# Performance work log

Measured on AMD Instinct MI355X. Metric: run time of the kernel, lower is better.

Reference implementation:

```python
import jax, jax.numpy as jnp
import numpy as np

N, E, H, L = 20000, 640000, 128, 3
IN_NODE, IN_EDGE = 128, 128


def _ln(x):
    m = jnp.mean(x, -1, keepdims=True)
    v = jnp.mean((x - m) ** 2, -1, keepdims=True)
    return (x - m) / jnp.sqrt(v + 1e-5)


def _multi_aggr(msg, dst, n):
    # PyG MultiAggregation(['mean','std','max','min']) -> concat on feature dim
    cnt = jax.ops.segment_sum(jnp.ones((msg.shape[0],), msg.dtype), dst, n)
    denom = jnp.maximum(cnt, 1.0)[:, None]
    mean = jax.ops.segment_sum(msg, dst, n) / denom
    mean2 = jax.ops.segment_sum(msg * msg, dst, n) / denom
    std = jnp.sqrt(jax.nn.relu(mean2 - mean * mean) + 1e-5)  # PyG StdAggregation
    has = (cnt > 0)[:, None]
    mx = jnp.where(has, jax.ops.segment_max(msg, dst, n), 0.0)
    mn = jnp.where(has, jax.ops.segment_min(msg, dst, n), 0.0)
    return jnp.concatenate([mean, std, mx, mn], axis=-1)  # [n, 4H]


def _pna(h, src, dst, ea, W1, b1, W2, b2, W3, b3, W4, b4, Wd, bd, n):
    # flow='source_to_target': j = src = edge_index[0], i = dst = edge_index[1]
    x1 = jax.nn.silu(h @ W1 + b1)  # lin1 -> x_j
    z = jax.nn.silu(h @ W2 + b2)   # lin2 -> z_i
    msg = z[dst] * x1[src] * ea    # message = z_i * x_j * edge_attr
    ret_node = _multi_aggr(msg, dst, n) @ Wd + bd
    ret_edge = jax.nn.silu(h @ W3 + b3)[src] * jax.nn.silu(h @ W4 + b4)[dst] * ea
    return ret_node, ret_edge


def _gnn(x, edge_index, edge_attr, Wn, bn, We, be, W1, b1, W2, b2, W3, b3, W4, b4,
         Wd, bd, Wnd1, bnd1, Wnd2, bnd2, Wed1, bed1, Wed2, bed2):
    n = x.shape[0]
    h = Wn.shape[1]
    src, dst = edge_index[0], edge_index[1]
    inv = jnp.concatenate([jnp.ones((h // 2,), x.dtype), -jnp.ones(((h + 1) // 2,), x.dtype)])
    hidden = x @ Wn + bn
    in_ea = edge_attr
    ea = edge_attr @ We + be
    for i in range(W1.shape[0]):
        hn = _ln(hidden)
        rn1, re1 = _pna(hn, src, dst, ea, W1[i], b1[i], W2[i], b2[i], W3[i], b3[i], W4[i], b4[i], Wd[i], bd[i], n)
        rn2, re2 = _pna(hn, dst, src, inv * ea, W1[i], b1[i], W2[i], b2[i], W3[i], b3[i], W4[i], b4[i], Wd[i], bd[i], n)
        hidden = hidden + rn1 + rn2
        ea = ea + re1 + inv * re2
    node_pred = x + 0.01 * (jax.nn.silu(_ln(hidden) @ Wnd1 + bnd1) @ Wnd2 + bnd2)
    edge_pred = in_ea + 0.01 * (jax.nn.silu(_ln(ea) @ Wed1 + bed1) @ Wed2 + bed2)
    return node_pred, edge_pred


def setup_inputs() -> dict:
    key = jax.random.key(0)
    ks = jax.random.split(key, 20)
    g = lambda k, s, sc=0.05: jax.random.normal(k, s, jnp.float32) * sc
    return {
        "x": g(ks[0], (N, IN_NODE), 1.0),
        "edge_attr": g(ks[1], (E, IN_EDGE), 1.0),
        "Wn": g(ks[2], (IN_NODE, H)), "bn": jnp.zeros((H,), jnp.float32),
        "We": g(ks[3], (IN_EDGE, H)), "be": jnp.zeros((H,), jnp.float32),
        "W1": g(ks[4], (L, H, H)), "b1": jnp.zeros((L, H), jnp.float32),
        "W2": g(ks[5], (L, H, H)), "b2": jnp.zeros((L, H), jnp.float32),
        "W3": g(ks[6], (L, H, H)), "b3": jnp.zeros((L, H), jnp.float32),
        "W4": g(ks[7], (L, H, H)), "b4": jnp.zeros((L, H), jnp.float32),
        "Wd": g(ks[8], (L, 4 * H, H)), "bd": jnp.zeros((L, H), jnp.float32),
        "Wnd1": g(ks[9], (H, H)), "bnd1": jnp.zeros((H,), jnp.float32),
        "Wnd2": g(ks[10], (H, IN_NODE)), "bnd2": jnp.zeros((IN_NODE,), jnp.float32),
        "Wed1": g(ks[11], (H, H)), "bed1": jnp.zeros((H,), jnp.float32),
        "Wed2": g(ks[12], (H, IN_EDGE)), "bed2": jnp.zeros((IN_EDGE,), jnp.float32),
        "edge_index": jax.random.randint(ks[13], (2, E), 0, N),
    }


def reference(x, edge_attr, Wn, bn, We, be, W1, b1, W2, b2, W3, b3, W4, b4, Wd, bd,
              Wnd1, bnd1, Wnd2, bnd2, Wed1, bed1, Wed2, bed2, edge_index):
    return _gnn(x, edge_index, edge_attr, Wn, bn, We, be, W1, b1, W2, b2, W3, b3,
                W4, b4, Wd, bd, Wnd1, bnd1, Wnd2, bnd2, Wed1, bed1, Wed2, bed2)
```

## Files before the change

kernel.cpp:

```cpp
#include <hip/hip_runtime.h>
#include <cstdint>
#include <cstddef>

typedef __attribute__((ext_vector_type(8))) short short8x;
typedef __attribute__((ext_vector_type(4))) float f32x4;
typedef __attribute__((ext_vector_type(4))) unsigned int u32x4;

static constexpr int NN = 20000;
static constexpr int EE = 640000;
static constexpr int NT_E = EE / 128;

#define DEVI __device__ __forceinline__

DEVI float b2f(uint16_t u){ union{uint32_t i; float f;} x; x.i = (uint32_t)u<<16; return x.f; }
DEVI uint16_t f2b(float f){ union{float f; uint32_t i;} x; x.f=f; uint32_t i=x.i;
  return (uint16_t)((i + 0x7FFFu + ((i>>16)&1u))>>16); }
DEVI float silu_f(float v){ return v / (1.f + __expf(-v)); }

DEVI uint4 pack8(float4 a, float4 b){
  union{uint16_t u[8]; uint4 q;} pk;
  pk.u[0]=f2b(a.x); pk.u[1]=f2b(a.y); pk.u[2]=f2b(a.z); pk.u[3]=f2b(a.w);
  pk.u[4]=f2b(b.x); pk.u[5]=f2b(b.y); pk.u[6]=f2b(b.z); pk.u[7]=f2b(b.w);
  return pk.q;
}
DEVI uint2 pack4(float4 a){
  union{uint16_t u[4]; uint2 q;} pk;
  pk.u[0]=f2b(a.x); pk.u[1]=f2b(a.y); pk.u[2]=f2b(a.z); pk.u[3]=f2b(a.w);
  return pk.q;
}
DEVI float4 unpk4(uint2 v){
  return (float4){ b2f((uint16_t)(v.x & 0xFFFFu)), b2f((uint16_t)(v.x >> 16)),
                   b2f((uint16_t)(v.y & 0xFFFFu)), b2f((uint16_t)(v.y >> 16)) };
}
DEVI short8x pk_frag(float4 a, float4 b){
  union{uint16_t u[8]; short8x s;} pk;
  pk.u[0]=f2b(a.x); pk.u[1]=f2b(a.y); pk.u[2]=f2b(a.z); pk.u[3]=f2b(a.w);
  pk.u[4]=f2b(b.x); pk.u[5]=f2b(b.y); pk.u[6]=f2b(b.z); pk.u[7]=f2b(b.w);
  return pk.s;
}

DEVI float4 ntld4f(const float* p){
  f32x4 v = __builtin_nontemporal_load((const f32x4*)p);
  return (float4){v.x, v.y, v.z, v.w};
}

template<typename EAT>
DEVI void load8e(const EAT* base, size_t row, int col8, float4& a, float4& b){
  if constexpr (sizeof(EAT)==2){
    uint4 v = *(const uint4*)((const uint16_t*)base + row*128 + col8);
    a = (float4){b2f((uint16_t)(v.x&0xFFFFu)), b2f((uint16_t)(v.x>>16)),
                 b2f((uint16_t)(v.y&0xFFFFu)), b2f((uint16_t)(v.y>>16))};
    b = (float4){b2f((uint16_t)(v.z&0xFFFFu)), b2f((uint16_t)(v.z>>16)),
                 b2f((uint16_t)(v.w&0xFFFFu)), b2f((uint16_t)(v.w>>16))};
  } else {
    const float* f = (const float*)base + row*128 + col8;
    a = *(const float4*)f; b = *(const float4*)(f+4);
  }
}
template<typename EAT>
DEVI void store4e(EAT* base, size_t idx, float4 v){
  if constexpr (sizeof(EAT)==2) *(uint2*)((uint16_t*)base + idx) = pack4(v);
  else *(float4*)((float*)base + idx) = v;
}
template<typename EAT>
DEVI float4 ld4e(const EAT* base, size_t idx){
  if constexpr (sizeof(EAT)==2) return unpk4(*(const uint2*)((const uint16_t*)base + idx));
  else return *(const float4*)((const float*)base + idx);
}

DEVI void ln8(float4& a, float4& b){
  float s = a.x+a.y+a.z+a.w + b.x+b.y+b.z+b.w;
  float q = a.x*a.x+a.y*a.y+a.z*a.z+a.w*a.w + b.x*b.x+b.y*b.y+b.z*b.z+b.w*b.w;
#pragma unroll
  for (int d=1; d<16; d<<=1){ s += __shfl_xor(s,d); q += __shfl_xor(q,d); }
  float m = s * 0.0078125f;
  float rstd = rsqrtf(fmaxf(q*0.0078125f - m*m, 0.f) + 1e-5f);
  a.x=(a.x-m)*rstd; a.y=(a.y-m)*rstd; a.z=(a.z-m)*rstd; a.w=(a.w-m)*rstd;
  b.x=(b.x-m)*rstd; b.y=(b.y-m)*rstd; b.z=(b.z-m)*rstd; b.w=(b.w-m)*rstd;
}

template<int AF32, int LNA, int EPI, int SILU>
__global__ __launch_bounds__(256) void gemm_node(
    const void* Ap, const uint16_t* __restrict__ Wt,
    const float* __restrict__ bias, float bias_scale,
    int M, int K,
    uint16_t* outb, float* outf,
    const float* __restrict__ resid, float resid_scale)
{
  __shared__ uint16_t Als[128*136];
  __shared__ uint16_t Wls[128*136];
  const int t = threadIdx.x;
  const int row0 = blockIdx.x * 128;
  const int w = t >> 6, l = t & 63;
  const int lr = l & 15, lk = (l>>4)*8;

  f32x4 acc[2][8];
#pragma unroll
  for (int a=0;a<2;a++)
#pragma unroll
    for(int b=0;b<8;b++) acc[a][b] = (f32x4){0.f,0.f,0.f,0.f};

  for (int kc = 0; kc < K; kc += 128){
#pragma unroll
    for (int i=0;i<8;i++){
      int c = t + i*256;
      int r = c >> 4, k8 = (c & 15)*8;
      int gr = row0 + r;
      if (AF32){
        float4 a = {0.f,0.f,0.f,0.f}, b = {0.f,0.f,0.f,0.f};
        if (gr < M){
          const float* Af = (const float*)Ap + (size_t)gr*K + kc + k8;
          a = *(const float4*)Af; b = *(const float4*)(Af + 4);
        }
        if (LNA) ln8(a, b);
        *(uint4*)(&Als[r*136 + k8]) = pack8(a, b);
      } else {
        uint4 v = {0u,0u,0u,0u};
        if (gr < M) v = *(const uint4*)((const uint16_t*)Ap + (size_t)gr*K + kc + k8);
        *(uint4*)(&Als[r*136 + k8]) = v;
      }
    }
#pragma unroll
    for (int i=0;i<8;i++){
      int c = t + i*256;
      int r = c >> 4, k8 = (c & 15)*8;
      *(uint4*)(&Wls[r*136 + k8]) = *(const uint4*)(Wt + (size_t)r*K + kc + k8);
    }
    __syncthreads();
#pragma unroll
    for (int kt=0; kt<4; ++kt){
      int kb = kt*32 + lk;
      short8x bfr[8];
#pragma unroll
      for (int c16=0;c16<8;c16++) bfr[c16] = *(const short8x*)(&Wls[(c16*16+lr)*136 + kb]);
#pragma unroll
      for (int r16=0;r16<2;r16++){
        short8x afr = *(const short8x*)(&Als[(w*32 + r16*16 + lr)*136 + kb]);
#pragma unroll
        for (int c16=0;c16<8;c16++)
          acc[r16][c16] = __builtin_amdgcn_mfma_f32_16x16x32_bf16(bfr[c16], afr, acc[r16][c16], 0,0,0);
      }
    }
    __syncthreads();
  }

  float4 bbv[8];
#pragma unroll
  for (int c16=0;c16<8;c16++){
    float4 b4 = *(const float4*)(bias + c16*16 + (l>>4)*4);
    bbv[c16] = (float4){b4.x*bias_scale, b4.y*bias_scale, b4.z*bias_scale, b4.w*bias_scale};
  }
#pragma unroll
  for (int r16=0;r16<2;r16++){
    int row = row0 + w*32 + r16*16 + lr;
    if (row >= M) continue;
#pragma unroll
    for (int c16=0;c16<8;c16++){
      int colb = c16*16 + (l>>4)*4;
      float4 v = (float4){acc[r16][c16][0]+bbv[c16].x, acc[r16][c16][1]+bbv[c16].y,
                          acc[r16][c16][2]+bbv[c16].z, acc[r16][c16][3]+bbv[c16].w};
      if (SILU){ v.x=silu_f(v.x); v.y=silu_f(v.y); v.z=silu_f(v.z); v.w=silu_f(v.w); }
      size_t o = (size_t)row*128 + colb;
      if (EPI==0)      *(uint2*)(outb + o) = pack4(v);
      else if (EPI==1) *(float4*)(outf + o) = v;
      else if (EPI==2){ float4 old = *(const float4*)(outf + o);
        *(float4*)(outf + o) = (float4){old.x+v.x, old.y+v.y, old.z+v.z, old.w+v.w}; }
      else { float4 r = *(const float4*)(resid + o);
        *(float4*)(outf + o) = (float4){r.x+resid_scale*v.x, r.y+resid_scale*v.y,
                                        r.z+resid_scale*v.z, r.w+resid_scale*v.w}; }
    }
  }
}

__global__ __launch_bounds__(256) void proj4(
    const float* __restrict__ hidden, const uint16_t* __restrict__ Wt4,
    const float* __restrict__ b0p, const float* __restrict__ b1p,
    const float* __restrict__ b2p, const float* __restrict__ b3p,
    uint16_t* o0, uint16_t* o1, uint16_t* o2, uint16_t* o3, int M)
{
  __shared__ uint16_t Als[128*136];
  __shared__ uint16_t Wls[2][128*136];
  const int t = threadIdx.x;
  const int row0 = blockIdx.x * 128;
  const int w = t >> 6, l = t & 63;
  const int lr = l & 15, lk = (l>>4)*8;

#pragma unroll
  for (int i=0;i<8;i++){
    int c = t + i*256;
    int r = c >> 4, k8 = (c & 15)*8;
    int gr = row0 + r;
    float4 a = {0.f,0.f,0.f,0.f}, b = {0.f,0.f,0.f,0.f};
    if (gr < M){
      const float* Af = hidden + (size_t)gr*128 + k8;
      a = *(const float4*)Af; b = *(const float4*)(Af + 4);
    }
    ln8(a, b);
    *(uint4*)(&Als[r*136 + k8]) = pack8(a, b);
  }
#pragma unroll
  for (int i=0;i<8;i++){
    int c = t + i*256;
    int r = c >> 4, k8 = (c & 15)*8;
    *(uint4*)(&Wls[0][r*136 + k8]) = *(const uint4*)(Wt4 + (size_t)r*128 + k8);
  }
  __syncthreads();

#pragma unroll
  for (int p=0; p<4; ++p){
    if (p < 3){
#pragma unroll
      for (int i=0;i<8;i++){
        int c = t + i*256;
        int r = c >> 4, k8 = (c & 15)*8;
        *(uint4*)(&Wls[(p+1)&1][r*136 + k8]) =
          *(const uint4*)(Wt4 + (size_t)(p+1)*16384 + (size_t)r*128 + k8);
      }
    }
    f32x4 acc[2][8];
#pragma unroll
    for (int a=0;a<2;a++)
#pragma unroll
      for(int b=0;b<8;b++) acc[a][b] = (f32x4){0.f,0.f,0.f,0.f};
#pragma unroll
    for (int kt=0; kt<4; ++kt){
      int kb = kt*32 + lk;
      short8x bfr[8];
#pragma unroll
      for (int c16=0;c16<8;c16++) bfr[c16] = *(const short8x*)(&Wls[p&1][(c16*16+lr)*136 + kb]);
#pragma unroll
      for (int r16=0;r16<2;r16++){
        short8x afr = *(const short8x*)(&Als[(w*32 + r16*16 + lr)*136 + kb]);
#pragma unroll
        for (int c16=0;c16<8;c16++)
          acc[r16][c16] = __builtin_amdgcn_mfma_f32_16x16x32_bf16(bfr[c16], afr, acc[r16][c16], 0,0,0);
      }
    }
    const float* bp = (p==0)?b0p:(p==1)?b1p:(p==2)?b2p:b3p;
    uint16_t* op = (p==0)?o0:(p==1)?o1:(p==2)?o2:o3;
#pragma unroll
    for (int r16=0;r16<2;r16++){
      int row = row0 + w*32 + r16*16 + lr;
      if (row >= M) continue;
#pragma unroll
      for (int c16=0;c16<8;c16++){
        int colb = c16*16 + (l>>4)*4;
        float4 b4 = *(const float4*)(bp + colb);
        float4 v = (float4){silu_f(acc[r16][c16][0]+b4.x), silu_f(acc[r16][c16][1]+b4.y),
                            silu_f(acc[r16][c16][2]+b4.z), silu_f(acc[r16][c16][3]+b4.w)};
        *(uint2*)(op + (size_t)row*128 + colb) = pack4(v);
      }
    }
    __syncthreads();
  }
}

template<typename EAT>
__global__ __launch_bounds__(256, 2) void enc_edge(
    const float* __restrict__ A, const uint16_t* __restrict__ Wt,
    const float* __restrict__ bias, EAT* __restrict__ out)
{
  const int t = threadIdx.x, w = t >> 6, l = t & 63;
  const int lr = l & 15, g = l >> 4;

  float4 bbv[8];
#pragma unroll
  for (int c16=0;c16<8;c16++) bbv[c16] = *(const float4*)(bias + c16*16 + g*4);

  int tile = blockIdx.x;
  float4 va[16];
#pragma unroll
  for (int r16=0;r16<2;r16++)
#pragma unroll
    for (int kt=0;kt<4;kt++){
      const float* Af = A + ((size_t)tile*128 + w*32 + r16*16 + lr)*128 + kt*32 + g*8;
      va[r16*8+kt*2]   = ntld4f(Af);
      va[r16*8+kt*2+1] = ntld4f(Af + 4);
    }
  while (tile < NT_E){
    short8x fr[2][4];
#pragma unroll
    for (int r16=0;r16<2;r16++)
#pragma unroll
      for (int kt=0;kt<4;kt++)
        fr[r16][kt] = pk_frag(va[r16*8+kt*2], va[r16*8+kt*2+1]);
    int next = tile + (int)gridDim.x;
    if (next < NT_E){
#pragma unroll
      for (int r16=0;r16<2;r16++)
#pragma unroll
        for (int kt=0;kt<4;kt++){
          const float* Af = A + ((size_t)next*128 + w*32 + r16*16 + lr)*128 + kt*32 + g*8;
          va[r16*8+kt*2]   = ntld4f(Af);
          va[r16*8+kt*2+1] = ntld4f(Af + 4);
        }
    }
    f32x4 acc[2][8];
#pragma unroll
    for (int a=0;a<2;a++)
#pragma unroll
      for (int b=0;b<8;b++) acc[a][b] = (f32x4){0.f,0.f,0.f,0.f};
#pragma unroll
    for (int kt=0;kt<4;kt++){
#pragma unroll
      for (int c16=0;c16<8;c16++){
        short8x bfr = *(const short8x*)(Wt + (size_t)(c16*16+lr)*128 + kt*32 + g*8);
        acc[0][c16] = __builtin_amdgcn_mfma_f32_16x16x32_bf16(bfr, fr[0][kt], acc[0][c16], 0,0,0);
        acc[1][c16] = __builtin_amdgcn_mfma_f32_16x16x32_bf16(bfr, fr[1][kt], acc[1][c16], 0,0,0);
      }
    }
#pragma unroll
    for (int r16=0;r16<2;r16++){
      size_t row = (size_t)tile*128 + w*32 + r16*16 + lr;
#pragma unroll
      for (int c16=0;c16<8;c16++){
        int colb = c16*16 + g*4;
        store4e(out, row*128 + colb,
          (float4){acc[r16][c16][0]+bbv[c16].x, acc[r16][c16][1]+bbv[c16].y,
                   acc[r16][c16][2]+bbv[c16].z, acc[r16][c16][3]+bbv[c16].w});
      }
    }
    tile = next;
  }
}

template<typename EAT>
__global__ __launch_bounds__(256, 2) void dec_edge(
    const EAT* ea, const float* __restrict__ eatt,
    const uint16_t* __restrict__ W1t, const uint16_t* __restrict__ W2t,
    const float* __restrict__ b1, const float* __restrict__ b2,
    float* outf)
{
  __shared__ uint16_t Pls[4][32*136];
  const int t = threadIdx.x, w = t >> 6, l = t & 63;
  const int lr = l & 15, g = l >> 4;
  uint16_t* Ps = &Pls[w][0];
  const size_t base = (size_t)blockIdx.x*128 + w*32;

  float4 et[16];
#pragma unroll
  for (int r16=0;r16<2;r16++){
    size_t row = base + r16*16 + lr;
#pragma unroll
    for (int c16=0;c16<8;c16++)
      et[r16*8+c16] = *(const float4*)(eatt + row*128 + c16*16 + g*4);
  }

  short8x fr[2][4];
#pragma unroll
  for (int r16=0;r16<2;r16++){
    float4 va[4][2];
    float s=0.f, q=0.f;
#pragma unroll
    for (int kt=0;kt<4;kt++){
      load8e(ea, base + r16*16 + lr, kt*32 + g*8, va[kt][0], va[kt][1]);
      float4 a = va[kt][0], b = va[kt][1];
      s += a.x+a.y+a.z+a.w + b.x+b.y+b.z+b.w;
      q += a.x*a.x+a.y*a.y+a.z*a.z+a.w*a.w + b.x*b.x+b.y*b.y+b.z*b.z+b.w*b.w;
    }
    s += __shfl_xor(s,16); q += __shfl_xor(q,16);
    s += __shfl_xor(s,32); q += __shfl_xor(q,32);
    float m = s*0.0078125f;
    float rstd = rsqrtf(fmaxf(q*0.0078125f - m*m, 0.f) + 1e-5f);
#pragma unroll
    for (int kt=0;kt<4;kt++){
      float4 a = va[kt][0], b = va[kt][1];
      a.x=(a.x-m)*rstd; a.y=(a.y-m)*rstd; a.z=(a.z-m)*rstd; a.w=(a.w-m)*rstd;
      b.x=(b.x-m)*rstd; b.y=(b.y-m)*rstd; b.z=(b.z-m)*rstd; b.w=(b.w-m)*rstd;
      fr[r16][kt] = pk_frag(a, b);
    }
  }
  f32x4 acc[2][8];
#pragma unroll
  for (int a=0;a<2;a++)
#pragma unroll
    for (int b=0;b<8;b++) acc[a][b] = (f32x4){0.f,0.f,0.f,0.f};
#pragma unroll
  for (int kt=0;kt<4;kt++){
#pragma unroll
    for (int c16=0;c16<8;c16++){
      short8x bfr = *(const short8x*)(W1t + (size_t)(c16*16+lr)*128 + kt*32 + g*8);
      acc[0][c16] = __builtin_amdgcn_mfma_f32_16x16x32_bf16(fr[0][kt], bfr, acc[0][c16], 0,0,0);
      acc[1][c16] = __builtin_amdgcn_mfma_f32_16x16x32_bf16(fr[1][kt], bfr, acc[1][c16], 0,0,0);
    }
  }
#pragma unroll
  for (int c16=0;c16<8;c16++){
    float bb = b1[c16*16+lr];
#pragma unroll
    for (int r16=0;r16<2;r16++)
#pragma unroll
      for (int j=0;j<4;j++)
        Ps[(r16*16 + g*4 + j)*136 + c16*16 + lr] = f2b(silu_f(acc[r16][c16][j] + bb));
  }
  f32x4 acc2[2][8];
#pragma unroll
  for (int a=0;a<2;a++)
#pragma unroll
    for (int b=0;b<8;b++) acc2[a][b] = (f32x4){0.f,0.f,0.f,0.f};
#pragma unroll
  for (int kt=0;kt<4;kt++){
    short8x a0 = *(const short8x*)(Ps + (0*16 + lr)*136 + kt*32 + g*8);
    short8x a1 = *(const short8x*)(Ps + (1*16 + lr)*136 + kt*32 + g*8);
#pragma unroll
    for (int c16=0;c16<8;c16++){
      short8x bfr = *(const short8x*)(W2t + (size_t)(c16*16+lr)*128 + kt*32 + g*8);
      acc2[0][c16] = __builtin_amdgcn_mfma_f32_16x16x32_bf16(bfr, a0, acc2[0][c16], 0,0,0);
      acc2[1][c16] = __builtin_amdgcn_mfma_f32_16x16x32_bf16(bfr, a1, acc2[1][c16], 0,0,0);
    }
  }
#pragma unroll
  for (int r16=0;r16<2;r16++){
    size_t row = base + r16*16 + lr;
#pragma unroll
    for (int c16=0;c16<8;c16++){
      int colb = c16*16 + g*4;
      float4 bb = *(const float4*)(b2 + colb);
      float4 e = et[r16*8+c16];
      *(float4*)(outf + row*128 + colb) =
        (float4){e.x + 0.01f*(acc2[r16][c16][0]+bb.x),
                 e.y + 0.01f*(acc2[r16][c16][1]+bb.y),
                 e.z + 0.01f*(acc2[r16][c16][2]+bb.z),
                 e.w + 0.01f*(acc2[r16][c16][3]+bb.w)};
    }
  }
}

template<typename EAT, int INV, int EUPD, int ACCUM>
__global__ __launch_bounds__(128) void agg_kernel(
    const EAT* ea, EAT* ea_out,
    const uint16_t* __restrict__ x1, const uint16_t* __restrict__ z,
    const uint16_t* __restrict__ h3, const uint16_t* __restrict__ h4,
    const int* __restrict__ eids, const int* __restrict__ ptr,
    const int* __restrict__ other, uint16_t* stats)
{
  __shared__ int se[128];
  __shared__ int so[128];
  __shared__ float red[4][4][128];
  const int i = blockIdx.x, t = threadIdx.x;
  const int g = t >> 5, q = t & 31;
  const int f0 = q*4;
  float4 zi = unpk4(*(const uint2*)(z + (size_t)i*128 + f0));
  float4 h3i = {0,0,0,0}, h4i = {0,0,0,0};
  if (EUPD){
    h3i = unpk4(*(const uint2*)(h3 + (size_t)i*128 + f0));
    h4i = unpk4(*(const uint2*)(h4 + (size_t)i*128 + f0));
  }
  const int beg = ptr[i], end = ptr[i+1];
  float4 s={0,0,0,0}, s2={0,0,0,0};
  float4 mx={-3.4e38f,-3.4e38f,-3.4e38f,-3.4e38f}, mn={3.4e38f,3.4e38f,3.4e38f,3.4e38f};
  for (int jb = beg; jb < end; jb += 128){
    int cn = min(128, end - jb);
    if (t < cn){ int e = eids[jb+t]; se[t] = e; so[t] = other[e]; }
    __syncthreads();
#pragma unroll 4
    for (int jj = g; jj < cn; jj += 4){
      int e = se[jj], o = so[jj];
      float4 xo = unpk4(*(const uint2*)(x1 + (size_t)o*128 + f0));
      float4 ev = ld4e(ea, (size_t)e*128 + f0);
      float4 m = (float4){zi.x*xo.x*ev.x, zi.y*xo.y*ev.y, zi.z*xo.z*ev.z, zi.w*xo.w*ev.w};
      if (INV){ if (q >= 16){ m.x=-m.x; m.y=-m.y; m.z=-m.z; m.w=-m.w; } }
      s.x+=m.x; s.y+=m.y; s.z+=m.z; s.w+=m.w;
      s2.x+=m.x*m.x; s2.y+=m.y*m.y; s2.z+=m.z*m.z; s2.w+=m.w*m.w;
      mx.x=fmaxf(mx.x,m.x); mx.y=fmaxf(mx.y,m.y); mx.z=fmaxf(mx.z,m.z); mx.w=fmaxf(mx.w,m.w);
      mn.x=fminf(mn.x,m.x); mn.y=fminf(mn.y,m.y); mn.z=fminf(mn.z,m.z); mn.w=fminf(mn.w,m.w);
      if (EUPD){
        float4 h3o = unpk4(*(const uint2*)(h3 + (size_t)o*128 + f0));
        float4 h4o = unpk4(*(const uint2*)(h4 + (size_t)o*128 + f0));
        store4e(ea_out, (size_t)e*128 + f0,
          (float4){ev.x*(1.f + h3o.x*h4i.x + h3i.x*h4o.x),
                   ev.y*(1.f + h3o.y*h4i.y + h3i.y*h4o.y),
                   ev.z*(1.f + h3o.z*h4i.z + h3i.z*h4o.z),
                   ev.w*(1.f + h3o.w*h4i.w + h3i.w*h4o.w)});
      }
    }
    __syncthreads();
  }
  *(float4*)(&red[g][0][f0]) = s;
  *(float4*)(&red[g][1][f0]) = s2;
  *(float4*)(&red[g][2][f0]) = mx;
  *(float4*)(&red[g][3][f0]) = mn;
  __syncthreads();
  float fs = red[0][0][t]+red[1][0][t]+red[2][0][t]+red[3][0][t];
  float fq = red[0][1][t]+red[1][1][t]+red[2][1][t]+red[3][1][t];
  float fmx = fmaxf(fmaxf(red[0][2][t],red[1][2][t]), fmaxf(red[2][2][t],red[3][2][t]));
  float fmn = fminf(fminf(red[0][3][t],red[1][3][t]), fminf(red[2][3][t],red[3][3][t]));
  int cnt = end - beg;
  float dn = cnt > 0 ? 1.f/(float)cnt : 1.f;
  float mean = fs*dn, m2 = fq*dn;
  float sd = sqrtf(fmaxf(m2 - mean*mean, 0.f) + 1e-5f);
  if (cnt == 0){ fmx = 0.f; fmn = 0.f; }
  size_t o0 = (size_t)i*512 + t;
  if (ACCUM){
    stats[o0    ] = f2b(b2f(stats[o0    ]) + mean);
    stats[o0+128] = f2b(b2f(stats[o0+128]) + sd);
    stats[o0+256] = f2b(b2f(stats[o0+256]) + fmx);
    stats[o0+384] = f2b(b2f(stats[o0+384]) + fmn);
  } else {
    stats[o0]=f2b(mean); stats[o0+128]=f2b(sd); stats[o0+256]=f2b(fmx); stats[o0+384]=f2b(fmn);
  }
}

__global__ void count_deg(const int* __restrict__ ei, int* cnt_src, int* cnt_dst){
  int e = blockIdx.x*256 + threadIdx.x;
  if (e < EE){
    atomicAdd(&cnt_src[ei[e]], 1);
    atomicAdd(&cnt_dst[ei[EE+e]], 1);
  }
}

__global__ __launch_bounds__(1024) void scan20k(const int* __restrict__ cnt, int* ptr, int* cur){
  __shared__ int buf[1024];
  constexpr int C = 20;
  int t = threadIdx.x;
  int base = t*C;
  int loc[C];
  int sum = 0;
#pragma unroll
  for (int j=0;j<C;j++){
    int idx = base+j;
    int v = (idx < NN) ? cnt[idx] : 0;
    loc[j] = sum; sum += v;
  }
  buf[t] = sum;
  __syncthreads();
  for (int sft=1; sft<1024; sft<<=1){
    int add = (t>=sft) ? buf[t-sft] : 0;
    __syncthreads();
    buf[t] += add;
    __syncthreads();
  }
  int excl = buf[t] - sum;
#pragma unroll
  for (int j=0;j<C;j++){
    int idx = base+j;
    if (idx < NN){ int v = excl + loc[j]; ptr[idx] = v; cur[idx] = v; }
  }
  if (t == 1023) ptr[NN] = buf[1023];
}

__global__ void scatter_edges(const int* __restrict__ ei, int* cur_src, int* cur_dst,
                              int* eid_src, int* eid_dst){
  int e = blockIdx.x*256 + threadIdx.x;
  if (e < EE){
    int s = ei[e], d = ei[EE+e];
    eid_src[atomicAdd(&cur_src[s],1)] = e;
    eid_dst[atomicAdd(&cur_dst[d],1)] = e;
  }
}

struct TD { const float* s; uint16_t* d; int K; int ostride; int ooff; int cum; };
struct TPack { TD td[11]; };
__global__ __launch_bounds__(256) void transpose_all(TPack P, int total){
  int idx = blockIdx.x*256 + threadIdx.x;
  if (idx >= total) return;
  int s = 0;
#pragma unroll
  for (int k=0;k<11;k++) s += (idx >= P.td[k].cum) ? 1 : 0;
  int start = (s==0) ? 0 : P.td[s-1].cum;
  int local = idx - start;
  const TD& D = P.td[s];
  int per = D.K*128;
  int m = local / per, r = local - m*per;
  int k = r >> 7, c = r & 127;
  D.d[(size_t)m*D.ostride + D.ooff + (size_t)c*D.K + k] = f2b(D.s[local]);
}

extern "C" void kernel_launch(void* const* d_in, const int* in_sizes, int n_in,
                              void* d_out, int out_size, void* d_ws, size_t ws_size,
                              hipStream_t stream)
{
  const float* x    = (const float*)d_in[0];
  const float* eatt = (const float*)d_in[1];
  const float* Wn   = (const float*)d_in[2];
  const float* bn   = (const float*)d_in[3];
  const float* We   = (const float*)d_in[4];
  const float* be   = (const float*)d_in[5];
  const float* W1   = (const float*)d_in[6];
  const float* b1   = (const float*)d_in[7];
  const float* W2   = (const float*)d_in[8];
  const float* b2   = (const float*)d_in[9];
  const float* W3   = (const float*)d_in[10];
  const float* b3   = (const float*)d_in[11];
  const float* W4   = (const float*)d_in[12];
  const float* b4   = (const float*)d_in[13];
  const float* Wd   = (const float*)d_in[14];
  const float* bd   = (const float*)d_in[15];
  const float* Wnd1 = (const float*)d_in[16];
  const float* bnd1 = (const float*)d_in[17];
  const float* Wnd2 = (const float*)d_in[18];
  const float* bnd2 = (const float*)d_in[19];
  const float* Wed1 = (const float*)d_in[20];
  const float* bed1 = (const float*)d_in[21];
  const float* Wed2 = (const float*)d_in[22];
  const float* bed2 = (const float*)d_in[23];
  const int* ei     = (const int*)d_in[24];

  float* out_node = (float*)d_out;
  float* out_edge = out_node + (size_t)NN*128;

  char* p = (char*)d_ws;
  auto alloc = [&](size_t bytes)->char*{
    char* r = p; p += (bytes + 255) & ~(size_t)255; return r; };

  float*    hidden = (float*)   alloc((size_t)NN*128*4);
  uint16_t* x1b    = (uint16_t*)alloc((size_t)NN*128*2);
  uint16_t* zb     = (uint16_t*)alloc((size_t)NN*128*2);
  uint16_t* h3b    = (uint16_t*)alloc((size_t)NN*128*2);
  uint16_t* h4b    = (uint16_t*)alloc((size_t)NN*128*2);
  uint16_t* stats  = (uint16_t*)alloc((size_t)NN*512*2);
  int* cnt_src = (int*)alloc((size_t)NN*4);
  int* cnt_dst = (int*)alloc((size_t)NN*4);
  int* ptr_src = (int*)alloc((size_t)(NN+1)*4);
  int* ptr_dst = (int*)alloc((size_t)(NN+1)*4);
  int* cur_src = (int*)alloc((size_t)NN*4);
  int* cur_dst = (int*)alloc((size_t)NN*4);
  int* eid_src = (int*)alloc((size_t)EE*4);
  int* eid_dst = (int*)alloc((size_t)EE*4);
  uint16_t* WT  = (uint16_t*)alloc((size_t)294912*2);
  uint16_t* wp4 = (uint16_t*)alloc((size_t)3*65536*2);

  uint16_t* wnT   = WT;
  uint16_t* weT   = WT + 16384;
  uint16_t* wdT   = WT + 32768;
  uint16_t* wnd1T = WT + 229376;
  uint16_t* wnd2T = WT + 245760;
  uint16_t* wed1T = WT + 262144;
  uint16_t* wed2T = WT + 278528;

  size_t used = (size_t)(p - (char*)d_ws);
  bool ea16ok = (ws_size >= used + (size_t)EE*128*2 + 512);
  uint16_t* ea16 = nullptr;
  if (ea16ok) ea16 = (uint16_t*)alloc((size_t)EE*128*2);
  float* eaf = out_edge;

  hipMemsetAsync(cnt_src, 0, (size_t)NN*4, stream);
  hipMemsetAsync(cnt_dst, 0, (size_t)NN*4, stream);
  count_deg<<<(EE+255)/256, 256, 0, stream>>>(ei, cnt_src, cnt_dst);
  scan20k<<<1, 1024, 0, stream>>>(cnt_src, ptr_src, cur_src);
  scan20k<<<1, 1024, 0, stream>>>(cnt_dst, ptr_dst, cur_dst);
  scatter_edges<<<(EE+255)/256, 256, 0, stream>>>(ei, cur_src, cur_dst, eid_src, eid_dst);

  {
    TPack P;
    int cum = 0;
    auto seg = [&](int idx, const float* s, uint16_t* d, int K, int total, int ostride, int ooff){
      cum += total;
      P.td[idx] = TD{s, d, K, ostride, ooff, cum};
    };
    seg(0,  Wn,   wnT,   128, 16384,  16384, 0);
    seg(1,  We,   weT,   128, 16384,  16384, 0);
    seg(2,  W1,   wp4,   128, 49152,  65536, 0);
    seg(3,  W2,   wp4,   128, 49152,  65536, 16384);
    seg(4,  W3,   wp4,   128, 49152,  65536, 32768);
    seg(5,  W4,   wp4,   128, 49152,  65536, 49152);
    seg(6,  Wd,   wdT,   512, 196608, 65536, 0);
    seg(7,  Wnd1, wnd1T, 128, 16384,  16384, 0);
    seg(8,  Wnd2, wnd2T, 128, 16384,  16384, 0);
    seg(9,  Wed1, wed1T, 128, 16384,  16384, 0);
    seg(10, Wed2, wed2T, 128, 16384,  16384, 0);
    transpose_all<<<(cum+255)/256, 256, 0, stream>>>(P, cum);
  }

  const int gN = (NN+127)/128;

  gemm_node<1,0,1,0><<<gN, 256, 0, stream>>>(x, wnT, bn, 1.f, NN, 128, nullptr, hidden, nullptr, 0.f);

  if (ea16ok){
    enc_edge<uint16_t><<<1000, 256, 0, stream>>>(eatt, weT, be, ea16);
    for (int lyr = 0; lyr < 3; ++lyr){
      proj4<<<gN, 256, 0, stream>>>(hidden, wp4 + (size_t)lyr*65536,
                                    b1 + lyr*128, b2 + lyr*128, b3 + lyr*128, b4 + lyr*128,
                                    x1b, zb, h3b, h4b, NN);
      agg_kernel<uint16_t,1,0,0><<<NN, 128, 0, stream>>>(ea16, nullptr, x1b, zb, nullptr, nullptr,
                                                         eid_src, ptr_src, ei + EE, stats);
      agg_kernel<uint16_t,0,1,1><<<NN, 128, 0, stream>>>(ea16, ea16, x1b, zb, h3b, h4b,
                                                         eid_dst, ptr_dst, ei, stats);
      gemm_node<0,0,2,0><<<gN, 256, 0, stream>>>(stats, wdT + lyr*65536, bd + lyr*128, 2.f,
                                                 NN, 512, nullptr, hidden, nullptr, 0.f);
    }
  } else {
    enc_edge<float><<<1000, 256, 0, stream>>>(eatt, weT, be, eaf);
    for (int lyr = 0; lyr < 3; ++lyr){
      proj4<<<gN, 256, 0, stream>>>(hidden, wp4 + (size_t)lyr*65536,
                                    b1 + lyr*128, b2 + lyr*128, b3 + lyr*128, b4 + lyr*128,
                                    x1b, zb, h3b, h4b, NN);
      agg_kernel<float,1,0,0><<<NN, 128, 0, stream>>>(eaf, nullptr, x1b, zb, nullptr, nullptr,
                                                      eid_src, ptr_src, ei + EE, stats);
      agg_kernel<float,0,1,1><<<NN, 128, 0, stream>>>(eaf, eaf, x1b, zb, h3b, h4b,
                                                      eid_dst, ptr_dst, ei, stats);
      gemm_node<0,0,2,0><<<gN, 256, 0, stream>>>(stats, wdT + lyr*65536, bd + lyr*128, 2.f,
                                                 NN, 512, nullptr, hidden, nullptr, 0.f);
    }
  }

  gemm_node<1,1,0,1><<<gN, 256, 0, stream>>>(hidden, wnd1T, bnd1, 1.f, NN, 128, x1b, nullptr, nullptr, 0.f);
  gemm_node<0,0,3,0><<<gN, 256, 0, stream>>>(x1b, wnd2T, bnd2, 1.f, NN, 128, nullptr, out_node, x, 0.01f);

  if (ea16ok)
    dec_edge<uint16_t><<<NT_E, 256, 0, stream>>>(ea16, eatt, wed1T, wed2T, bed1, bed2, out_edge);
  else
    dec_edge<float><<<NT_E, 256, 0, stream>>>(eaf, eatt, wed1T, wed2T, bed1, bed2, out_edge);
}
```

Baseline: 1.425 ms.

## Make dec_edge persistent with register prefetch of next tile inputs

The edge decoder becomes a grid-stride persistent kernel launched with 1024 blocks instead of one block per 128-edge tile. Each iteration loads the next tile's edge features and edge attributes into registers while the current tile's MFMA GEMMs run, and the biases are hoisted out of the loop. The aim is to hide global load latency and cut block launch overhead. In exchange, register pressure rises from holding prefetched data, which could lower occupancy or cause spills under the 256x2 launch bounds.

```diff
diff --git a/kernel.cpp b/kernel.cpp
--- a/kernel.cpp
+++ b/kernel.cpp
@@ -4,7 +4,6 @@
 
 typedef __attribute__((ext_vector_type(8))) short short8x;
 typedef __attribute__((ext_vector_type(4))) float f32x4;
-typedef __attribute__((ext_vector_type(4))) unsigned int u32x4;
 
 static constexpr int NN = 20000;
 static constexpr int EE = 640000;
@@ -32,6 +31,12 @@
   return (float4){ b2f((uint16_t)(v.x & 0xFFFFu)), b2f((uint16_t)(v.x >> 16)),
                    b2f((uint16_t)(v.y & 0xFFFFu)), b2f((uint16_t)(v.y >> 16)) };
 }
+DEVI void unpk8(uint4 v, float4& a, float4& b){
+  a = (float4){b2f((uint16_t)(v.x&0xFFFFu)), b2f((uint16_t)(v.x>>16)),
+               b2f((uint16_t)(v.y&0xFFFFu)), b2f((uint16_t)(v.y>>16))};
+  b = (float4){b2f((uint16_t)(v.z&0xFFFFu)), b2f((uint16_t)(v.z>>16)),
+               b2f((uint16_t)(v.w&0xFFFFu)), b2f((uint16_t)(v.w>>16))};
+}
 DEVI short8x pk_frag(float4 a, float4 b){
   union{uint16_t u[8]; short8x s;} pk;
   pk.u[0]=f2b(a.x); pk.u[1]=f2b(a.y); pk.u[2]=f2b(a.z); pk.u[3]=f2b(a.w);
@@ -44,19 +49,6 @@
   return (float4){v.x, v.y, v.z, v.w};
 }
 
-template<typename EAT>
-DEVI void load8e(const EAT* base, size_t row, int col8, float4& a, float4& b){
-  if constexpr (sizeof(EAT)==2){
-    uint4 v = *(const uint4*)((const uint16_t*)base + row*128 + col8);
-    a = (float4){b2f((uint16_t)(v.x&0xFFFFu)), b2f((uint16_t)(v.x>>16)),
-                 b2f((uint16_t)(v.y&0xFFFFu)), b2f((uint16_t)(v.y>>16))};
-    b = (float4){b2f((uint16_t)(v.z&0xFFFFu)), b2f((uint16_t)(v.z>>16)),
-                 b2f((uint16_t)(v.w&0xFFFFu)), b2f((uint16_t)(v.w>>16))};
-  } else {
-    const float* f = (const float*)base + row*128 + col8;
-    a = *(const float4*)f; b = *(const float4*)(f+4);
-  }
-}
 template<typename EAT>
 DEVI void store4e(EAT* base, size_t idx, float4 v){
   if constexpr (sizeof(EAT)==2) *(uint2*)((uint16_t*)base + idx) = pack4(v);
@@ -335,94 +327,153 @@
   const int t = threadIdx.x, w = t >> 6, l = t & 63;
   const int lr = l & 15, g = l >> 4;
   uint16_t* Ps = &Pls[w][0];
-  const size_t base = (size_t)blockIdx.x*128 + w*32;
-
+
+  float bb1[8];
+  float4 bb2v[8];
+#pragma unroll
+  for (int c16=0;c16<8;c16++){
+    bb1[c16] = b1[c16*16+lr];
+    bb2v[c16] = *(const float4*)(b2 + c16*16 + g*4);
+  }
+
+  int tile = blockIdx.x;
+  size_t base = (size_t)tile*128 + w*32;
+
+  uint4 eaR[8];
+  float4 eaF[16];
   float4 et[16];
-#pragma unroll
-  for (int r16=0;r16<2;r16++){
-    size_t row = base + r16*16 + lr;
-#pragma unroll
-    for (int c16=0;c16<8;c16++)
-      et[r16*8+c16] = *(const float4*)(eatt + row*128 + c16*16 + g*4);
-  }
-
-  short8x fr[2][4];
-#pragma unroll
-  for (int r16=0;r16<2;r16++){
-    float4 va[4][2];
-    float s=0.f, q=0.f;
+
+  if (tile < NT_E){
+    if constexpr (sizeof(EAT)==2){
+#pragma unroll
+      for (int r16=0;r16<2;r16++)
+#pragma unroll
+        for (int kt=0;kt<4;kt++)
+          eaR[r16*4+kt] = *(const uint4*)((const uint16_t*)ea + (base + r16*16+lr)*128 + kt*32 + g*8);
+    } else {
+#pragma unroll
+      for (int r16=0;r16<2;r16++)
+#pragma unroll
+        for (int kt=0;kt<4;kt++){
+          const float* f = (const float*)ea + (base + r16*16+lr)*128 + kt*32 + g*8;
+          eaF[(r16*4+kt)*2]   = *(const float4*)f;
+          eaF[(r16*4+kt)*2+1] = *(const float4*)(f+4);
+        }
+    }
+#pragma unroll
+    for (int r16=0;r16<2;r16++)
+#pragma unroll
+      for (int c16=0;c16<8;c16++)
+        et[r16*8+c16] = *(const float4*)(eatt + (base + r16*16+lr)*128 + c16*16 + g*4);
+  }
+
+  while (tile < NT_E){
+    short8x fr[2][4];
+#pragma unroll
+    for (int r16=0;r16<2;r16++){
+      float4 va[4][2];
+      float s=0.f, q=0.f;
+#pragma unroll
+      for (int kt=0;kt<4;kt++){
+        if constexpr (sizeof(EAT)==2) unpk8(eaR[r16*4+kt], va[kt][0], va[kt][1]);
+        else { va[kt][0]=eaF[(r16*4+kt)*2]; va[kt][1]=eaF[(r16*4+kt)*2+1]; }
+        float4 a = va[kt][0], b = va[kt][1];
+        s += a.x+a.y+a.z+a.w + b.x+b.y+b.z+b.w;
+        q += a.x*a.x+a.y*a.y+a.z*a.z+a.w*a.w + b.x*b.x+b.y*b.y+b.z*b.z+b.w*b.w;
+      }
+      s += __shfl_xor(s,16); q += __shfl_xor(q,16);
+      s += __shfl_xor(s,32); q += __shfl_xor(q,32);
+      float m = s*0.0078125f;
+      float rstd = rsqrtf(fmaxf(q*0.0078125f - m*m, 0.f) + 1e-5f);
+#pragma unroll
+      for (int kt=0;kt<4;kt++){
+        float4 a = va[kt][0], b = va[kt][1];
+        a.x=(a.x-m)*rstd; a.y=(a.y-m)*rstd; a.z=(a.z-m)*rstd; a.w=(a.w-m)*rstd;
+        b.x=(b.x-m)*rstd; b.y=(b.y-m)*rstd; b.z=(b.z-m)*rstd; b.w=(b.w-m)*rstd;
+        fr[r16][kt] = pk_frag(a, b);
+      }
+    }
+    int next = tile + (int)gridDim.x;
+    size_t nbase = (size_t)next*128 + w*32;
+    if (next < NT_E){
+      if constexpr (sizeof(EAT)==2){
+#pragma unroll
+        for (int r16=0;r16<2;r16++)
+#pragma unroll
+          for (int kt=0;kt<4;kt++)
+            eaR[r16*4+kt] = *(const uint4*)((const uint16_t*)ea + (nbase + r16*16+lr)*128 + kt*32 + g*8);
+      } else {
+#pragma unroll
+        for (int r16=0;r16<2;r16++)
+#pragma unroll
+          for (int kt=0;kt<4;kt++){
+            const float* f = (const float*)ea + (nbase + r16*16+lr)*128 + kt*32 + g*8;
+            eaF[(r16*4+kt)*2]   = *(const float4*)f;
+            eaF[(r16*4+kt)*2+1] = *(const float4*)(f+4);
+          }
+      }
+    }
+    f32x4 acc[2][8];
+#pragma unroll
+    for (int a=0;a<2;a++)
+#pragma unroll
+      for (int b=0;b<8;b++) acc[a][b] = (f32x4){0.f,0.f,0.f,0.f};
 #pragma unroll
     for (int kt=0;kt<4;kt++){
-      load8e(ea, base + r16*16 + lr, kt*32 + g*8, va[kt][0], va[kt][1]);
-      float4 a = va[kt][0], b = va[kt][1];
-      s += a.x+a.y+a.z+a.w + b.x+b.y+b.z+b.w;
-      q += a.x*a.x+a.y*a.y+a.z*a.z+a.w*a.w + b.x*b.x+b.y*b.y+b.z*b.z+b.w*b.w;
-    }
-    s += __shfl_xor(s,16); q += __shfl_xor(q,16);
-    s += __shfl_xor(s,32); q += __shfl_xor(q,32);
-    float m = s*0.0078125f;
-    float rstd = rsqrtf(fmaxf(q*0.0078125f - m*m, 0.f) + 1e-5f);
+#pragma unroll
+      for (int c16=0;c16<8;c16++){
+        short8x bfr = *(const short8x*)(W1t + (size_t)(c16*16+lr)*128 + kt*32 + g*8);
+        acc[0][c16] = __builtin_amdgcn_mfma_f32_16x16x32_bf16(fr[0][kt], bfr, acc[0][c16], 0,0,0);
+        acc[1][c16] = __builtin_amdgcn_mfma_f32_16x16x32_bf16(fr[1][kt], bfr, acc[1][c16], 0,0,0);
+      }
+    }
+#pragma unroll
+    for (int c16=0;c16<8;c16++){
+#pragma unroll
+      for (int r16=0;r16<2;r16++)
+#pragma unroll
+        for (int j=0;j<4;j++)
+          Ps[(r16*16 + g*4 + j)*136 + c16*16 + lr] = f2b(silu_f(acc[r16][c16][j] + bb1[c16]));
+    }
+    f32x4 acc2[2][8];
+#pragma unroll
+    for (int a=0;a<2;a++)
+#pragma unroll
+      for (int b=0;b<8;b++) acc2[a][b] = (f32x4){0.f,0.f,0.f,0.f};
 #pragma unroll
     for (int kt=0;kt<4;kt++){
-      float4 a = va[kt][0], b = va[kt][1];
-      a.x=(a.x-m)*rstd; a.y=(a.y-m)*rstd; a.z=(a.z-m)*rstd; a.w=(a.w-m)*rstd;
-      b.x=(b.x-m)*rstd; b.y=(b.y-m)*rstd; b.z=(b.z-m)*rstd; b.w=(b.w-m)*rstd;
-      fr[r16][kt] = pk_frag(a, b);
-    }
-  }
-  f32x4 acc[2][8];
-#pragma unroll
-  for (int a=0;a<2;a++)
-#pragma unroll
-    for (int b=0;b<8;b++) acc[a][b] = (f32x4){0.f,0.f,0.f,0.f};
-#pragma unroll
-  for (int kt=0;kt<4;kt++){
-#pragma unroll
-    for (int c16=0;c16<8;c16++){
-      short8x bfr = *(const short8x*)(W1t + (size_t)(c16*16+lr)*128 + kt*32 + g*8);
-      acc[0][c16] = __builtin_amdgcn_mfma_f32_16x16x32_bf16(fr[0][kt], bfr, acc[0][c16], 0,0,0);
-      acc[1][c16] = __builtin_amdgcn_mfma_f32_16x16x32_bf16(fr[1][kt], bfr, acc[1][c16], 0,0,0);
-    }
-  }
-#pragma unroll
-  for (int c16=0;c16<8;c16++){
-    float bb = b1[c16*16+lr];
-#pragma unroll
-    for (int r16=0;r16<2;r16++)
-#pragma unroll
-      for (int j=0;j<4;j++)
-        Ps[(r16*16 + g*4 + j)*136 + c16*16 + lr] = f2b(silu_f(acc[r16][c16][j] + bb));
-  }
-  f32x4 acc2[2][8];
-#pragma unroll
-  for (int a=0;a<2;a++)
-#pragma unroll
-    for (int b=0;b<8;b++) acc2[a][b] = (f32x4){0.f,0.f,0.f,0.f};
-#pragma unroll
-  for (int kt=0;kt<4;kt++){
-    short8x a0 = *(const short8x*)(Ps + (0*16 + lr)*136 + kt*32 + g*8);
-    short8x a1 = *(const short8x*)(Ps + (1*16 + lr)*136 + kt*32 + g*8);
-#pragma unroll
-    for (int c16=0;c16<8;c16++){
-      short8x bfr = *(const short8x*)(W2t + (size_t)(c16*16+lr)*128 + kt*32 + g*8);
-      acc2[0][c16] = __builtin_amdgcn_mfma_f32_16x16x32_bf16(bfr, a0, acc2[0][c16], 0,0,0);
-      acc2[1][c16] = __builtin_amdgcn_mfma_f32_16x16x32_bf16(bfr, a1, acc2[1][c16], 0,0,0);
-    }
-  }
-#pragma unroll
-  for (int r16=0;r16<2;r16++){
-    size_t row = base + r16*16 + lr;
-#pragma unroll
-    for (int c16=0;c16<8;c16++){
-      int colb = c16*16 + g*4;
-      float4 bb = *(const float4*)(b2 + colb);
-      float4 e = et[r16*8+c16];
-      *(float4*)(outf + row*128 + colb) =
-        (float4){e.x + 0.01f*(acc2[r16][c16][0]+bb.x),
-                 e.y + 0.01f*(acc2[r16][c16][1]+bb.y),
-                 e.z + 0.01f*(acc2[r16][c16][2]+bb.z),
-                 e.w + 0.01f*(acc2[r16][c16][3]+bb.w)};
-    }
+      short8x a0 = *(const short8x*)(Ps + (0*16 + lr)*136 + kt*32 + g*8);
+      short8x a1 = *(const short8x*)(Ps + (1*16 + lr)*136 + kt*32 + g*8);
+#pragma unroll
+      for (int c16=0;c16<8;c16++){
+        short8x bfr = *(const short8x*)(W2t + (size_t)(c16*16+lr)*128 + kt*32 + g*8);
+        acc2[0][c16] = __builtin_amdgcn_mfma_f32_16x16x32_bf16(bfr, a0, acc2[0][c16], 0,0,0);
+        acc2[1][c16] = __builtin_amdgcn_mfma_f32_16x16x32_bf16(bfr, a1, acc2[1][c16], 0,0,0);
+      }
+    }
+#pragma unroll
+    for (int r16=0;r16<2;r16++){
+      size_t row = base + r16*16 + lr;
+#pragma unroll
+      for (int c16=0;c16<8;c16++){
+        int colb = c16*16 + g*4;
+        float4 e = et[r16*8+c16];
+        *(float4*)(outf + row*128 + colb) =
+          (float4){e.x + 0.01f*(acc2[r16][c16][0]+bb2v[c16].x),
+                   e.y + 0.01f*(acc2[r16][c16][1]+bb2v[c16].y),
+                   e.z + 0.01f*(acc2[r16][c16][2]+bb2v[c16].z),
+                   e.w + 0.01f*(acc2[r16][c16][3]+bb2v[c16].w)};
+      }
+    }
+    if (next < NT_E){
+#pragma unroll
+      for (int r16=0;r16<2;r16++)
+#pragma unroll
+        for (int c16=0;c16<8;c16++)
+          et[r16*8+c16] = *(const float4*)(eatt + (nbase + r16*16+lr)*128 + c16*16 + g*4);
+    }
+    tile = next;
+    base = nbase;
   }
 }
 
@@ -698,7 +749,7 @@
   gemm_node<0,0,3,0><<<gN, 256, 0, stream>>>(x1b, wnd2T, bnd2, 1.f, NN, 128, nullptr, out_node, x, 0.01f);
 
   if (ea16ok)
-    dec_edge<uint16_t><<<NT_E, 256, 0, stream>>>(ea16, eatt, wed1T, wed2T, bed1, bed2, out_edge);
+    dec_edge<uint16_t><<<1024, 256, 0, stream>>>(ea16, eatt, wed1T, wed2T, bed1, bed2, out_edge);
   else
-    dec_edge<float><<<NT_E, 256, 0, stream>>>(eaf, eatt, wed1T, wed2T, bed1, bed2, out_edge);
-}
+    dec_edge<float><<<1024, 256, 0, stream>>>(eaf, eatt, wed1T, wed2T, bed1, bed2, out_edge);
+}
```

Result: slower. 1.626 ms (+14.1%).
